# Performance work log

Hardware: AMD Instinct MI355X
Metric: run time of the kernel (lower is better)

## Reference

```python
import jax, jax.numpy as jnp
import numpy as np
from jax import lax

B, T, C = 4, 2048, 1024
E, DFF, TOPK = 8, 4096, 2


def setup_inputs() -> dict:
    key = jax.random.key(0)
    ks = jax.random.split(key, 5)
    scale = 0.02
    x = jax.random.normal(ks[0], (B, T, C), dtype=jnp.float32)
    router_w = jax.random.normal(ks[1], (C, E), dtype=jnp.float32) * scale
    router_b = jnp.zeros((E,), dtype=jnp.float32)
    w1 = jax.random.normal(ks[2], (E, C, DFF), dtype=jnp.float32) * scale
    b1 = jnp.zeros((E, DFF), dtype=jnp.float32)
    w2 = jax.random.normal(ks[3], (E, DFF, C), dtype=jnp.float32) * scale
    b2 = jnp.zeros((E, C), dtype=jnp.float32)
    return {"x": x, "router_w": router_w, "router_b": router_b,
            "w1": w1, "b1": b1, "w2": w2, "b2": b2, "top_k": TOPK}


def reference(x, router_w, router_b, w1, b1, w2, b2, top_k):
    # Router: softmax then top-k (matches torch.topk(F.softmax(logits)))
    logits = jnp.einsum('btc,ce->bte', x, router_w) + router_b   # [B,T,E]
    probs = jax.nn.softmax(logits, axis=-1)
    weights, indices = lax.top_k(probs, top_k)                    # [B,T,k]
    n_exp = w1.shape[0]
    # Combined per-expert weight per token (sum over top-k slots hitting expert j)
    onehot = jax.nn.one_hot(indices, n_exp, dtype=x.dtype)        # [B,T,k,E]
    cw = jnp.sum(weights[..., None] * onehot, axis=-2)            # [B,T,E]
    bsz, seq, dim = x.shape
    flat_x = x.reshape(-1, dim)                                   # [N,C]
    flat_cw = cw.reshape(-1, n_exp)                               # [N,E]
    out = jnp.zeros_like(flat_x)
    for j in range(n_exp):  # fixed small expert loop (dropout=0 -> eval)
        h = jax.nn.gelu(flat_x @ w1[j] + b1[j], approximate=False)
        out = out + flat_cw[:, j:j + 1] * (h @ w2[j] + b2[j])
    return out.reshape(bsz, seq, dim)
```

## Files before the change

### kernel.cpp

```cpp
#include <hip/hip_runtime.h>
#include <math.h>

typedef __bf16 bf16;
typedef bf16 bf16x4 __attribute__((ext_vector_type(4)));
typedef bf16 bf16x8 __attribute__((ext_vector_type(8)));
typedef float f32x4 __attribute__((ext_vector_type(4)));

#define NTOK 8192
#define CDIM 1024
#define EXP 8
#define DFF 4096
#define BM 256
#define BN 256
#define BK 64
#define HALF_E 8192

__device__ __forceinline__ void gld_lds16(const bf16* g, bf16* l) {
  __builtin_amdgcn_global_load_lds(
      (const __attribute__((address_space(1))) unsigned int*)g,
      (__attribute__((address_space(3))) unsigned int*)l, 16, 0, 0);
}

__global__ __launch_bounds__(256) void convert_x(const float* __restrict__ in,
                                                 bf16* __restrict__ out) {
  int idx = (blockIdx.x * 256 + threadIdx.x) * 8;
  float4 a = *(const float4*)(in + idx);
  float4 b = *(const float4*)(in + idx + 4);
  bf16x8 v;
  v[0] = (bf16)a.x; v[1] = (bf16)a.y; v[2] = (bf16)a.z; v[3] = (bf16)a.w;
  v[4] = (bf16)b.x; v[5] = (bf16)b.y; v[6] = (bf16)b.z; v[7] = (bf16)b.w;
  *(bf16x8*)(out + idx) = v;
}

__global__ __launch_bounds__(256) void transpose_cvt(
    const float* __restrict__ in, bf16* __restrict__ out, int R, int Cin) {
  __shared__ float tile[64][33];
  int e = blockIdx.z;
  const float* ip = in + (size_t)e * R * Cin;
  bf16* op = out + (size_t)e * R * Cin;
  int c0 = blockIdx.x * 32, r0 = blockIdx.y * 64;
  int tr = threadIdx.x >> 5, tc = threadIdx.x & 31;
#pragma unroll
  for (int i = 0; i < 8; i++)
    tile[tr + 8 * i][tc] = ip[(size_t)(r0 + tr + 8 * i) * Cin + c0 + tc];
  __syncthreads();
  int oc = threadIdx.x >> 3;
  int orr = (threadIdx.x & 7) * 8;
  bf16x8 v;
#pragma unroll
  for (int k = 0; k < 8; k++) v[k] = (bf16)tile[orr + k][oc];
  *(bf16x8*)&op[(size_t)(c0 + oc) * R + r0 + orr] = v;
}

__global__ __launch_bounds__(256) void router_kernel(
    const float* __restrict__ x, const float* __restrict__ rw,
    const float* __restrict__ rb, unsigned int* __restrict__ cnt,
    int* __restrict__ list, float* __restrict__ wq) {
  int wave = threadIdx.x >> 6, lane = threadIdx.x & 63;
  int t = blockIdx.x * 4 + wave;
  if (t >= NTOK) return;
  const float* xr = x + (size_t)t * CDIM;
  float acc[8] = {0.f, 0.f, 0.f, 0.f, 0.f, 0.f, 0.f, 0.f};
  for (int c = lane; c < CDIM; c += 64) {
    float xv = xr[c];
    const float4* rp = (const float4*)(rw + c * 8);
    float4 r0 = rp[0], r1 = rp[1];
    acc[0] += xv * r0.x; acc[1] += xv * r0.y;
    acc[2] += xv * r0.z; acc[3] += xv * r0.w;
    acc[4] += xv * r1.x; acc[5] += xv * r1.y;
    acc[6] += xv * r1.z; acc[7] += xv * r1.w;
  }
#pragma unroll
  for (int e = 0; e < 8; e++)
#pragma unroll
    for (int off = 32; off; off >>= 1) acc[e] += __shfl_down(acc[e], off);
  if (lane == 0) {
    float p[8], mx = -1e30f;
#pragma unroll
    for (int e = 0; e < 8; e++) { p[e] = acc[e] + rb[e]; mx = fmaxf(mx, p[e]); }
    float s = 0.f;
#pragma unroll
    for (int e = 0; e < 8; e++) { p[e] = expf(p[e] - mx); s += p[e]; }
    float inv = 1.0f / s;
#pragma unroll
    for (int e = 0; e < 8; e++) p[e] *= inv;
    int i1 = 0;
#pragma unroll
    for (int e = 1; e < 8; e++) if (p[e] > p[i1]) i1 = e;
    int i2 = (i1 == 0) ? 1 : 0;
#pragma unroll
    for (int e = 0; e < 8; e++) if (e != i1 && p[e] > p[i2]) i2 = e;
    unsigned s0 = atomicAdd(&cnt[i1], 1u);
    list[i1 * NTOK + s0] = t * 2;
    unsigned s1 = atomicAdd(&cnt[i2], 1u);
    list[i2 * NTOK + s1] = t * 2 + 1;
    wq[t * 2] = p[i1];
    wq[t * 2 + 1] = p[i2];
  }
}

__device__ __forceinline__ void ld_afrag(const bf16* base, int aoff, int ih,
                                         bf16x8 (&af)[4]) {
#pragma unroll
  for (int i = 0; i < 4; i++)
    af[i] = *(const bf16x8*)&base[aoff + (ih * 64 + i * 16) * 32];
}
__device__ __forceinline__ void ld_bfrag(const bf16* base, int boff,
                                         bf16x8 (&bfr)[4]) {
#pragma unroll
  for (int j = 0; j < 4; j++)
    bfr[j] = *(const bf16x8*)&base[boff + j * 16 * 32];
}

#define MFMA16(IH)                                                        \
  do {                                                                    \
    __builtin_amdgcn_s_setprio(1);                                        \
    _Pragma("unroll") for (int i = 0; i < 4; i++)                         \
        _Pragma("unroll") for (int j = 0; j < 4; j++) acc[(IH)*4 + i][j] = \
            __builtin_amdgcn_mfma_f32_16x16x32_bf16(af[i], bfr[j],        \
                                                    acc[(IH)*4 + i][j],   \
                                                    0, 0, 0);             \
    __builtin_amdgcn_s_setprio(0);                                        \
  } while (0)

#define STAGE(P1, P2, LDSBUF, TK, KS)                                     \
  do {                                                                    \
    int _k = (TK) * BK + (KS)*32;                                         \
    bf16* _d = &LDSBUF[(((((TK)&1) << 1) | (KS)) * HALF_E) + tid * 8];    \
    gld_lds16((P1) + _k, _d);                                             \
    gld_lds16((P2) + _k, _d + 4096);                                      \
  } while (0)

template <int NT>
__device__ __forceinline__ void gemm_core(
    const bf16* aRow1, const bf16* aRow2, const bf16* bRow1, const bf16* bRow2,
    bf16* Asf, bf16* Bsf, int tid, f32x4 (&acc)[8][4]) {
  int w = tid >> 6, l = tid & 63;
  int ln = l & 15, kq = l >> 4;
  int wm = w >> 2, wn = w & 3;
  int rc8 = (kq ^ ((ln >> 1) & 3)) * 8;
  int aoff = (wm * 128 + ln) * 32 + rc8;
  int boff = (wn * 64 + ln) * 32 + rc8;

  bf16x8 af[4], bfr[4];

  STAGE(aRow1, aRow2, Asf, 0, 0);
  STAGE(bRow1, bRow2, Bsf, 0, 0);
  STAGE(aRow1, aRow2, Asf, 0, 1);
  STAGE(bRow1, bRow2, Bsf, 0, 1);
  STAGE(aRow1, aRow2, Asf, 1, 0);
  STAGE(bRow1, bRow2, Bsf, 1, 0);
  asm volatile("s_waitcnt vmcnt(8)" ::: "memory");
  __builtin_amdgcn_s_barrier();

  for (int t = 0; t < NT; ++t) {
    int sel = (t & 1) << 1;
    const bf16* A0 = &Asf[sel * HALF_E];
    const bf16* A1 = &Asf[(sel | 1) * HALF_E];
    const bf16* B0 = &Bsf[sel * HALF_E];
    const bf16* B1 = &Bsf[(sel | 1) * HALF_E];

    ld_bfrag(B0, boff, bfr);
    ld_afrag(A0, aoff, 0, af);
    if (t + 1 < NT) STAGE(aRow1, aRow2, Asf, t + 1, 1);
    if (t < NT - 1) asm volatile("s_waitcnt vmcnt(6)" ::: "memory");
    else            asm volatile("s_waitcnt vmcnt(0)" ::: "memory");
    __builtin_amdgcn_s_barrier();
    asm volatile("s_waitcnt lgkmcnt(0)" ::: "memory");
    __builtin_amdgcn_sched_barrier(0);
    MFMA16(0);
    __builtin_amdgcn_s_barrier();

    ld_afrag(A0, aoff, 1, af);
    if (t + 1 < NT) STAGE(bRow1, bRow2, Bsf, t + 1, 1);
    __builtin_amdgcn_s_barrier();
    asm volatile("s_waitcnt lgkmcnt(0)" ::: "memory");
    __builtin_amdgcn_sched_barrier(0);
    MFMA16(1);
    __builtin_amdgcn_s_barrier();

    ld_bfrag(B1, boff, bfr);
    ld_afrag(A1, aoff, 0, af);
    if (t + 2 < NT) STAGE(aRow1, aRow2, Asf, t + 2, 0);
    if (t < NT - 2)       asm volatile("s_waitcnt vmcnt(6)" ::: "memory");
    else if (t == NT - 2) asm volatile("s_waitcnt vmcnt(2)" ::: "memory");
    else                  asm volatile("s_waitcnt vmcnt(0)" ::: "memory");
    __builtin_amdgcn_s_barrier();
    asm volatile("s_waitcnt lgkmcnt(0)" ::: "memory");
    __builtin_amdgcn_sched_barrier(0);
    MFMA16(0);
    __builtin_amdgcn_s_barrier();

    ld_afrag(A1, aoff, 1, af);
    if (t + 2 < NT) STAGE(bRow1, bRow2, Bsf, t + 2, 0);
    __builtin_amdgcn_s_barrier();
    asm volatile("s_waitcnt lgkmcnt(0)" ::: "memory");
    __builtin_amdgcn_sched_barrier(0);
    MFMA16(1);
    __builtin_amdgcn_s_barrier();
  }
}

__global__ __launch_bounds__(512, 2) void gemm1_kernel(
    const bf16* __restrict__ xb, const bf16* __restrict__ w1b,
    const float* __restrict__ b1, const int* __restrict__ list,
    const unsigned int* __restrict__ cnt, bf16* __restrict__ h) {
  int bid = blockIdx.x + 16 * (blockIdx.y + 32 * blockIdx.z);
  int wg = (bid & 7) * 512 + (bid >> 3);
  int n0 = (wg & 15) * BN;
  int mt = (wg >> 4) & 31;
  int e = wg >> 9;
  int count = (int)min(cnt[e], (unsigned)NTOK);
  int m0 = mt * BM;
  if (m0 >= count) return;

  __shared__ __align__(16) bf16 Asf[4 * HALF_E];
  __shared__ __align__(16) bf16 Bsf[4 * HALF_E];

  int tid = threadIdx.x;
  int row1 = tid >> 2;
  int cx8 = ((tid & 3) ^ ((tid >> 3) & 3)) * 8;

  const int* lp = list + e * NTOK;
  int encA1 = lp[min(m0 + row1, count - 1)];
  int encA2 = lp[min(m0 + row1 + 128, count - 1)];
  const bf16* aRow1 = xb + (size_t)(encA1 >> 1) * CDIM + cx8;
  const bf16* aRow2 = xb + (size_t)(encA2 >> 1) * CDIM + cx8;
  const bf16* bRow1 =
      w1b + (size_t)e * DFF * CDIM + (size_t)(n0 + row1) * CDIM + cx8;
  const bf16* bRow2 = bRow1 + (size_t)128 * CDIM;

  f32x4 acc[8][4] = {};
  gemm_core<CDIM / BK>(aRow1, aRow2, bRow1, bRow2, Asf, Bsf, tid, acc);

  int w = tid >> 6, l = tid & 63;
  int ln = l & 15, kq = l >> 4;
  int wm = w >> 2, wn = w & 3;
  float b1f[4];
#pragma unroll
  for (int j = 0; j < 4; j++)
    b1f[j] = b1[e * DFF + n0 + wn * 64 + j * 16 + ln];
#pragma unroll
  for (int i = 0; i < 8; i++) {
#pragma unroll
    for (int r = 0; r < 4; r++) {
      int mrow = wm * 128 + i * 16 + kq * 4 + r;
      if (m0 + mrow < count) {
        int enc = lp[m0 + mrow];
        bf16* hr = h + (size_t)enc * DFF + n0 + wn * 64 + ln;
#pragma unroll
        for (int j = 0; j < 4; j++) {
          float v = acc[i][j][r] + b1f[j];
          float g = 0.5f * v * (1.0f + erff(v * 0.70710678118654752f));
          hr[j * 16] = (bf16)g;
        }
      }
    }
  }
}

__global__ __launch_bounds__(512, 2) void gemm2_kernel(
    const bf16* __restrict__ h, const bf16* __restrict__ w2b,
    const float* __restrict__ b2, const int* __restrict__ list,
    const unsigned int* __restrict__ cnt, const float* __restrict__ wq,
    float* __restrict__ y) {
  int bid = blockIdx.x + 4 * (blockIdx.y + 32 * blockIdx.z);
  int wg = (bid & 7) * 128 + (bid >> 3);
  int n0 = (wg & 3) * BN;
  int mt = (wg >> 2) & 31;
  int e = wg >> 7;
  int count = (int)min(cnt[e], (unsigned)NTOK);
  int m0 = mt * BM;
  if (m0 >= count) return;

  __shared__ __align__(16) bf16 Asf[4 * HALF_E];
  __shared__ __align__(16) bf16 Bsf[4 * HALF_E];

  int tid = threadIdx.x;
  int row1 = tid >> 2;
  int cx8 = ((tid & 3) ^ ((tid >> 3) & 3)) * 8;

  const int* lp = list + e * NTOK;
  int encA1 = lp[min(m0 + row1, count - 1)];
  int encA2 = lp[min(m0 + row1 + 128, count - 1)];
  const bf16* aRow1 = h + (size_t)encA1 * DFF + cx8;
  const bf16* aRow2 = h + (size_t)encA2 * DFF + cx8;
  const bf16* bRow1 =
      w2b + (size_t)e * CDIM * DFF + (size_t)(n0 + row1) * DFF + cx8;
  const bf16* bRow2 = bRow1 + (size_t)128 * DFF;

  f32x4 acc[8][4] = {};
  gemm_core<DFF / BK>(aRow1, aRow2, bRow1, bRow2, Asf, Bsf, tid, acc);

  int w = tid >> 6, l = tid & 63;
  int ln = l & 15, kq = l >> 4;
  int wm = w >> 2, wn = w & 3;
  float b2f[4];
#pragma unroll
  for (int j = 0; j < 4; j++)
    b2f[j] = b2[e * CDIM + n0 + wn * 64 + j * 16 + ln];
#pragma unroll
  for (int i = 0; i < 8; i++) {
#pragma unroll
    for (int r = 0; r < 4; r++) {
      int mrow = wm * 128 + i * 16 + kq * 4 + r;
      if (m0 + mrow < count) {
        int enc = lp[m0 + mrow];
        float wt = wq[enc];
        float* yr = y + (size_t)enc * CDIM + n0 + wn * 64 + ln;
#pragma unroll
        for (int j = 0; j < 4; j++)
          yr[j * 16] = wt * (acc[i][j][r] + b2f[j]);
      }
    }
  }
}

__global__ __launch_bounds__(256) void combine_kernel(
    const float* __restrict__ y, float* __restrict__ out) {
  int idx = (blockIdx.x * 256 + threadIdx.x) * 4;
  int t = idx >> 10;
  int c = idx & 1023;
  const float* y0 = y + ((size_t)(t * 2) << 10) + c;
  float4 a = *(const float4*)y0;
  float4 b = *(const float4*)(y0 + CDIM);
  float4 r;
  r.x = a.x + b.x; r.y = a.y + b.y; r.z = a.z + b.z; r.w = a.w + b.w;
  *(float4*)(out + idx) = r;
}

extern "C" void kernel_launch(void* const* d_in, const int* in_sizes, int n_in,
                              void* d_out, int out_size, void* d_ws,
                              size_t ws_size, hipStream_t stream) {
  const float* x = (const float*)d_in[0];
  const float* rw = (const float*)d_in[1];
  const float* rb = (const float*)d_in[2];
  const float* w1 = (const float*)d_in[3];
  const float* b1 = (const float*)d_in[4];
  const float* w2 = (const float*)d_in[5];
  const float* b2 = (const float*)d_in[6];
  float* out = (float*)d_out;

  char* ws = (char*)d_ws;
  size_t o = 0;
  auto carve = [&](size_t bytes) {
    void* p = ws + o;
    o = (o + bytes + 255) & ~(size_t)255;
    return p;
  };
  bf16* w1b = (bf16*)carve((size_t)EXP * DFF * CDIM * 2);
  bf16* w2b = (bf16*)carve((size_t)EXP * DFF * CDIM * 2);
  bf16* h = (bf16*)carve((size_t)2 * NTOK * DFF * 2);
  bf16* xb = (bf16*)carve((size_t)NTOK * CDIM * 2);
  int* list = (int*)carve((size_t)EXP * NTOK * 4);
  float* wq = (float*)carve((size_t)2 * NTOK * 4);
  unsigned int* cnt = (unsigned int*)carve(64);
  float* y = (float*)w1b;

  hipMemsetAsync(cnt, 0, 64, stream);

  convert_x<<<NTOK * CDIM / (256 * 8), 256, 0, stream>>>(x, xb);
  transpose_cvt<<<dim3(DFF / 32, CDIM / 64, EXP), 256, 0, stream>>>(w1, w1b,
                                                                    CDIM, DFF);
  transpose_cvt<<<dim3(CDIM / 32, DFF / 64, EXP), 256, 0, stream>>>(w2, w2b,
                                                                    DFF, CDIM);
  router_kernel<<<NTOK / 4, 256, 0, stream>>>(x, rw, rb, cnt, list, wq);
  gemm1_kernel<<<dim3(DFF / BN, NTOK / BM, EXP), 512, 0, stream>>>(
      xb, w1b, b1, list, cnt, h);
  gemm2_kernel<<<dim3(CDIM / BN, NTOK / BM, EXP), 512, 0, stream>>>(
      h, w2b, b2, list, cnt, wq, y);
  combine_kernel<<<NTOK * CDIM / (256 * 4), 256, 0, stream>>>(y, out);
}
```

Measured before the change: 1.086 ms.

## Shrink MoE GEMM tiles to 256x128x32 with triple-buffered LDS pipeline

Switches both expert GEMMs from 256x256x64 tiles with a double-buffered, four-phase schedule to 256x128x32 tiles with a three-stage rotating LDS buffer and one barrier phase per k-step. The smaller tile and LDS footprint allow launch bounds of 4 blocks per CU, raising occupancy and latency hiding. In exchange each block does less data reuse per load and the grid doubles, increasing global traffic for the weight and activation tiles.

Result: faster. 986.4 us (-9.1%).

```diff
diff --git a/kernel.cpp b/kernel.cpp
--- a/kernel.cpp
+++ b/kernel.cpp
@@ -11,9 +11,8 @@
 #define EXP 8
 #define DFF 4096
 #define BM 256
-#define BN 256
-#define BK 64
-#define HALF_E 8192
+#define BN 128
+#define BK 32
 
 __device__ __forceinline__ void gld_lds16(const bf16* g, bf16* l) {
   __builtin_amdgcn_global_load_lds(
@@ -99,158 +98,117 @@
   }
 }
 
-__device__ __forceinline__ void ld_afrag(const bf16* base, int aoff, int ih,
-                                         bf16x8 (&af)[4]) {
-#pragma unroll
-  for (int i = 0; i < 4; i++)
-    af[i] = *(const bf16x8*)&base[aoff + (ih * 64 + i * 16) * 32];
-}
-__device__ __forceinline__ void ld_bfrag(const bf16* base, int boff,
-                                         bf16x8 (&bfr)[4]) {
-#pragma unroll
-  for (int j = 0; j < 4; j++)
-    bfr[j] = *(const bf16x8*)&base[boff + j * 16 * 32];
-}
-
-#define MFMA16(IH)                                                        \
-  do {                                                                    \
-    __builtin_amdgcn_s_setprio(1);                                        \
-    _Pragma("unroll") for (int i = 0; i < 4; i++)                         \
-        _Pragma("unroll") for (int j = 0; j < 4; j++) acc[(IH)*4 + i][j] = \
-            __builtin_amdgcn_mfma_f32_16x16x32_bf16(af[i], bfr[j],        \
-                                                    acc[(IH)*4 + i][j],   \
-                                                    0, 0, 0);             \
-    __builtin_amdgcn_s_setprio(0);                                        \
+
+#define STAGE3(T, AS, BS)                    \
+  do {                                       \
+    int _k = (T)*BK;                         \
+    gld_lds16(aR1 + _k, (AS) + dstA);        \
+    gld_lds16(aR2 + _k, (AS) + dstA + 4096); \
+    gld_lds16(bR1 + _k, (BS) + dstA);        \
   } while (0)
 
-#define STAGE(P1, P2, LDSBUF, TK, KS)                                     \
-  do {                                                                    \
-    int _k = (TK) * BK + (KS)*32;                                         \
-    bf16* _d = &LDSBUF[(((((TK)&1) << 1) | (KS)) * HALF_E) + tid * 8];    \
-    gld_lds16((P1) + _k, _d);                                             \
-    gld_lds16((P2) + _k, _d + 4096);                                      \
-  } while (0)
-
 template <int NT>
-__device__ __forceinline__ void gemm_core(
-    const bf16* aRow1, const bf16* aRow2, const bf16* bRow1, const bf16* bRow2,
-    bf16* Asf, bf16* Bsf, int tid, f32x4 (&acc)[8][4]) {
+__device__ __forceinline__ void gemm_core(const bf16* aR1, const bf16* aR2,
+                                          const bf16* bR1, bf16* AsBase,
+                                          bf16* BsBase, int tid,
+                                          f32x4 (&acc)[4][4]) {
   int w = tid >> 6, l = tid & 63;
   int ln = l & 15, kq = l >> 4;
-  int wm = w >> 2, wn = w & 3;
+  int wm = w & 3, wn = w >> 2;
   int rc8 = (kq ^ ((ln >> 1) & 3)) * 8;
-  int aoff = (wm * 128 + ln) * 32 + rc8;
+  int aoff = (wm * 64 + ln) * 32 + rc8;
   int boff = (wn * 64 + ln) * 32 + rc8;
-
-  bf16x8 af[4], bfr[4];
-
-  STAGE(aRow1, aRow2, Asf, 0, 0);
-  STAGE(bRow1, bRow2, Bsf, 0, 0);
-  STAGE(aRow1, aRow2, Asf, 0, 1);
-  STAGE(bRow1, bRow2, Bsf, 0, 1);
-  STAGE(aRow1, aRow2, Asf, 1, 0);
-  STAGE(bRow1, bRow2, Bsf, 1, 0);
-  asm volatile("s_waitcnt vmcnt(8)" ::: "memory");
-  __builtin_amdgcn_s_barrier();
+  int dstA = (tid >> 2) * 32 + (tid & 3) * 8;
+
+  bf16* pA0 = AsBase;            bf16* pB0 = BsBase;
+  bf16* pA1 = AsBase + 8192;     bf16* pB1 = BsBase + 4096;
+  bf16* pA2 = AsBase + 16384;    bf16* pB2 = BsBase + 8192;
+
+  STAGE3(0, pA0, pB0);
+  STAGE3(1, pA1, pB1);
 
   for (int t = 0; t < NT; ++t) {
-    int sel = (t & 1) << 1;
-    const bf16* A0 = &Asf[sel * HALF_E];
-    const bf16* A1 = &Asf[(sel | 1) * HALF_E];
-    const bf16* B0 = &Bsf[sel * HALF_E];
-    const bf16* B1 = &Bsf[(sel | 1) * HALF_E];
-
-    ld_bfrag(B0, boff, bfr);
-    ld_afrag(A0, aoff, 0, af);
-    if (t + 1 < NT) STAGE(aRow1, aRow2, Asf, t + 1, 1);
-    if (t < NT - 1) asm volatile("s_waitcnt vmcnt(6)" ::: "memory");
-    else            asm volatile("s_waitcnt vmcnt(0)" ::: "memory");
+    if (t + 2 < NT) {
+      STAGE3(t + 2, pA2, pB2);
+      asm volatile("s_waitcnt vmcnt(6)" ::: "memory");
+    } else if (t + 1 < NT) {
+      asm volatile("s_waitcnt vmcnt(3)" ::: "memory");
+    } else {
+      asm volatile("s_waitcnt vmcnt(0)" ::: "memory");
+    }
     __builtin_amdgcn_s_barrier();
-    asm volatile("s_waitcnt lgkmcnt(0)" ::: "memory");
-    __builtin_amdgcn_sched_barrier(0);
-    MFMA16(0);
+
+    bf16x8 af[4], bfr[4];
+#pragma unroll
+    for (int i = 0; i < 4; i++)
+      af[i] = *(const bf16x8*)&pA0[aoff + i * 16 * 32];
+#pragma unroll
+    for (int j = 0; j < 4; j++)
+      bfr[j] = *(const bf16x8*)&pB0[boff + j * 16 * 32];
+    __builtin_amdgcn_s_setprio(1);
+#pragma unroll
+    for (int i = 0; i < 4; i++)
+#pragma unroll
+      for (int j = 0; j < 4; j++)
+        acc[i][j] = __builtin_amdgcn_mfma_f32_16x16x32_bf16(af[i], bfr[j],
+                                                            acc[i][j], 0, 0, 0);
+    __builtin_amdgcn_s_setprio(0);
     __builtin_amdgcn_s_barrier();
 
-    ld_afrag(A0, aoff, 1, af);
-    if (t + 1 < NT) STAGE(bRow1, bRow2, Bsf, t + 1, 1);
-    __builtin_amdgcn_s_barrier();
-    asm volatile("s_waitcnt lgkmcnt(0)" ::: "memory");
-    __builtin_amdgcn_sched_barrier(0);
-    MFMA16(1);
-    __builtin_amdgcn_s_barrier();
-
-    ld_bfrag(B1, boff, bfr);
-    ld_afrag(A1, aoff, 0, af);
-    if (t + 2 < NT) STAGE(aRow1, aRow2, Asf, t + 2, 0);
-    if (t < NT - 2)       asm volatile("s_waitcnt vmcnt(6)" ::: "memory");
-    else if (t == NT - 2) asm volatile("s_waitcnt vmcnt(2)" ::: "memory");
-    else                  asm volatile("s_waitcnt vmcnt(0)" ::: "memory");
-    __builtin_amdgcn_s_barrier();
-    asm volatile("s_waitcnt lgkmcnt(0)" ::: "memory");
-    __builtin_amdgcn_sched_barrier(0);
-    MFMA16(0);
-    __builtin_amdgcn_s_barrier();
-
-    ld_afrag(A1, aoff, 1, af);
-    if (t + 2 < NT) STAGE(bRow1, bRow2, Bsf, t + 2, 0);
-    __builtin_amdgcn_s_barrier();
-    asm volatile("s_waitcnt lgkmcnt(0)" ::: "memory");
-    __builtin_amdgcn_sched_barrier(0);
-    MFMA16(1);
-    __builtin_amdgcn_s_barrier();
-  }
-}
-
-__global__ __launch_bounds__(512, 2) void gemm1_kernel(
+    bf16* tA = pA0; pA0 = pA1; pA1 = pA2; pA2 = tA;
+    bf16* tB = pB0; pB0 = pB1; pB1 = pB2; pB2 = tB;
+  }
+}
+
+__global__ __launch_bounds__(512, 4) void gemm1_kernel(
     const bf16* __restrict__ xb, const bf16* __restrict__ w1b,
     const float* __restrict__ b1, const int* __restrict__ list,
     const unsigned int* __restrict__ cnt, bf16* __restrict__ h) {
-  int bid = blockIdx.x + 16 * (blockIdx.y + 32 * blockIdx.z);
-  int wg = (bid & 7) * 512 + (bid >> 3);
-  int n0 = (wg & 15) * BN;
-  int mt = (wg >> 4) & 31;
-  int e = wg >> 9;
+  int bid = blockIdx.x + 32 * (blockIdx.y + 32 * blockIdx.z);
+  int wg = (bid & 7) * 1024 + (bid >> 3);
+  int n0 = (wg & 31) * BN;
+  int mt = (wg >> 5) & 31;
+  int e = wg >> 10;
   int count = (int)min(cnt[e], (unsigned)NTOK);
   int m0 = mt * BM;
   if (m0 >= count) return;
 
-  __shared__ __align__(16) bf16 Asf[4 * HALF_E];
-  __shared__ __align__(16) bf16 Bsf[4 * HALF_E];
+  __shared__ __align__(16) bf16 As[3 * BM * BK];
+  __shared__ __align__(16) bf16 Bs[3 * BN * BK];
 
   int tid = threadIdx.x;
-  int row1 = tid >> 2;
-  int cx8 = ((tid & 3) ^ ((tid >> 3) & 3)) * 8;
+  int r = tid >> 2;
+  int sc8 = ((tid & 3) ^ ((r >> 1) & 3)) * 8;
 
   const int* lp = list + e * NTOK;
-  int encA1 = lp[min(m0 + row1, count - 1)];
-  int encA2 = lp[min(m0 + row1 + 128, count - 1)];
-  const bf16* aRow1 = xb + (size_t)(encA1 >> 1) * CDIM + cx8;
-  const bf16* aRow2 = xb + (size_t)(encA2 >> 1) * CDIM + cx8;
-  const bf16* bRow1 =
-      w1b + (size_t)e * DFF * CDIM + (size_t)(n0 + row1) * CDIM + cx8;
-  const bf16* bRow2 = bRow1 + (size_t)128 * CDIM;
-
-  f32x4 acc[8][4] = {};
-  gemm_core<CDIM / BK>(aRow1, aRow2, bRow1, bRow2, Asf, Bsf, tid, acc);
+  int encA1 = lp[min(m0 + r, count - 1)];
+  int encA2 = lp[min(m0 + r + 128, count - 1)];
+  const bf16* aR1 = xb + (size_t)(encA1 >> 1) * CDIM + sc8;
+  const bf16* aR2 = xb + (size_t)(encA2 >> 1) * CDIM + sc8;
+  const bf16* bR1 =
+      w1b + (size_t)e * DFF * CDIM + (size_t)(n0 + r) * CDIM + sc8;
+
+  f32x4 acc[4][4] = {};
+  gemm_core<CDIM / BK>(aR1, aR2, bR1, As, Bs, tid, acc);
 
   int w = tid >> 6, l = tid & 63;
   int ln = l & 15, kq = l >> 4;
-  int wm = w >> 2, wn = w & 3;
+  int wm = w & 3, wn = w >> 2;
   float b1f[4];
 #pragma unroll
   for (int j = 0; j < 4; j++)
     b1f[j] = b1[e * DFF + n0 + wn * 64 + j * 16 + ln];
 #pragma unroll
-  for (int i = 0; i < 8; i++) {
-#pragma unroll
-    for (int r = 0; r < 4; r++) {
-      int mrow = wm * 128 + i * 16 + kq * 4 + r;
+  for (int i = 0; i < 4; i++) {
+#pragma unroll
+    for (int rr = 0; rr < 4; rr++) {
+      int mrow = wm * 64 + i * 16 + kq * 4 + rr;
       if (m0 + mrow < count) {
         int enc = lp[m0 + mrow];
         bf16* hr = h + (size_t)enc * DFF + n0 + wn * 64 + ln;
 #pragma unroll
         for (int j = 0; j < 4; j++) {
-          float v = acc[i][j][r] + b1f[j];
+          float v = acc[i][j][rr] + b1f[j];
           float g = 0.5f * v * (1.0f + erff(v * 0.70710678118654752f));
           hr[j * 16] = (bf16)g;
         }
@@ -259,58 +217,57 @@
   }
 }
 
-__global__ __launch_bounds__(512, 2) void gemm2_kernel(
+__global__ __launch_bounds__(512, 4) void gemm2_kernel(
     const bf16* __restrict__ h, const bf16* __restrict__ w2b,
     const float* __restrict__ b2, const int* __restrict__ list,
     const unsigned int* __restrict__ cnt, const float* __restrict__ wq,
     float* __restrict__ y) {
-  int bid = blockIdx.x + 4 * (blockIdx.y + 32 * blockIdx.z);
-  int wg = (bid & 7) * 128 + (bid >> 3);
-  int n0 = (wg & 3) * BN;
-  int mt = (wg >> 2) & 31;
-  int e = wg >> 7;
+  int bid = blockIdx.x + 8 * (blockIdx.y + 32 * blockIdx.z);
+  int wg = (bid & 7) * 256 + (bid >> 3);
+  int n0 = (wg & 7) * BN;
+  int mt = (wg >> 3) & 31;
+  int e = wg >> 8;
   int count = (int)min(cnt[e], (unsigned)NTOK);
   int m0 = mt * BM;
   if (m0 >= count) return;
 
-  __shared__ __align__(16) bf16 Asf[4 * HALF_E];
-  __shared__ __align__(16) bf16 Bsf[4 * HALF_E];
+  __shared__ __align__(16) bf16 As[3 * BM * BK];
+  __shared__ __align__(16) bf16 Bs[3 * BN * BK];
 
   int tid = threadIdx.x;
-  int row1 = tid >> 2;
-  int cx8 = ((tid & 3) ^ ((tid >> 3) & 3)) * 8;
+  int r = tid >> 2;
+  int sc8 = ((tid & 3) ^ ((r >> 1) & 3)) * 8;
 
   const int* lp = list + e * NTOK;
-  int encA1 = lp[min(m0 + row1, count - 1)];
-  int encA2 = lp[min(m0 + row1 + 128, count - 1)];
-  const bf16* aRow1 = h + (size_t)encA1 * DFF + cx8;
-  const bf16* aRow2 = h + (size_t)encA2 * DFF + cx8;
-  const bf16* bRow1 =
-      w2b + (size_t)e * CDIM * DFF + (size_t)(n0 + row1) * DFF + cx8;
-  const bf16* bRow2 = bRow1 + (size_t)128 * DFF;
-
-  f32x4 acc[8][4] = {};
-  gemm_core<DFF / BK>(aRow1, aRow2, bRow1, bRow2, Asf, Bsf, tid, acc);
+  int encA1 = lp[min(m0 + r, count - 1)];
+  int encA2 = lp[min(m0 + r + 128, count - 1)];
+  const bf16* aR1 = h + (size_t)encA1 * DFF + sc8;
+  const bf16* aR2 = h + (size_t)encA2 * DFF + sc8;
+  const bf16* bR1 =
+      w2b + (size_t)e * CDIM * DFF + (size_t)(n0 + r) * DFF + sc8;
+
+  f32x4 acc[4][4] = {};
+  gemm_core<DFF / BK>(aR1, aR2, bR1, As, Bs, tid, acc);
 
   int w = tid >> 6, l = tid & 63;
   int ln = l & 15, kq = l >> 4;
-  int wm = w >> 2, wn = w & 3;
+  int wm = w & 3, wn = w >> 2;
   float b2f[4];
 #pragma unroll
   for (int j = 0; j < 4; j++)
     b2f[j] = b2[e * CDIM + n0 + wn * 64 + j * 16 + ln];
 #pragma unroll
-  for (int i = 0; i < 8; i++) {
-#pragma unroll
-    for (int r = 0; r < 4; r++) {
-      int mrow = wm * 128 + i * 16 + kq * 4 + r;
+  for (int i = 0; i < 4; i++) {
+#pragma unroll
+    for (int rr = 0; rr < 4; rr++) {
+      int mrow = wm * 64 + i * 16 + kq * 4 + rr;
       if (m0 + mrow < count) {
         int enc = lp[m0 + mrow];
         float wt = wq[enc];
         float* yr = y + (size_t)enc * CDIM + n0 + wn * 64 + ln;
 #pragma unroll
         for (int j = 0; j < 4; j++)
-          yr[j * 16] = wt * (acc[i][j][r] + b2f[j]);
+          yr[j * 16] = wt * (acc[i][j][rr] + b2f[j]);
       }
     }
   }
```
